# Performance work log

Measured on AMD Instinct MI355X. Metric: run time of the kernel, lower is better.

## Reference

```python
import jax, jax.numpy as jnp
import numpy as np

ALPHA, GAMMA = 0.25, 2.0
THR = 0.85            # soft_target_threshold
KL_EPS = 1e-6
FOCAL_EPS = 1e-8
VOC = 96              # len(vocab); index VOC is blank/pad


def setup_inputs() -> dict:
    key = jax.random.key(0)
    ks = jax.random.split(key, 6)
    bs, nq, n_pts, num_gt, L = 16, 200, 25, 32, 25
    return {
        "pred_logits": jax.random.normal(ks[0], (bs, nq, n_pts, 1), jnp.float32),
        "pred_ctrl_points": jax.random.uniform(ks[1], (bs, nq, n_pts, 2), jnp.float32),
        "pred_text_logits": jax.random.normal(ks[2], (bs, nq, n_pts, VOC + 1), jnp.float32),
        "tgt_ctrl_points": jax.random.uniform(ks[3], (bs, num_gt, n_pts, 2), jnp.float32),
        "tgt_texts": jax.random.randint(ks[4], (bs, num_gt, L), 0, VOC + 1),
        "centroids": jax.random.normal(ks[5], (VOC, 256), jnp.float32),
    }


def _cost_matrix(pred_logits, pred_ctrl_points, pred_text_logits,
                 tgt_ctrl_points, tgt_texts, centroids):
    bs, nq, n_pts, _ = pred_logits.shape
    num_gt = tgt_texts.shape[1]

    # ---- focal classification cost (mean over control points) ----
    out_prob = jax.nn.sigmoid(pred_logits.reshape(bs * nq, n_pts, -1))
    neg = (1.0 - ALPHA) * out_prob ** GAMMA * (-jnp.log1p(-(out_prob - FOCAL_EPS)))
    neg = (1.0 - ALPHA) * out_prob ** GAMMA * (-jnp.log(1.0 - out_prob + FOCAL_EPS))
    pos = ALPHA * (1.0 - out_prob) ** GAMMA * (-jnp.log(out_prob + FOCAL_EPS))
    cost_class = (pos[..., 0] - neg[..., 0]).mean(-1, keepdims=True)  # [bs*nq, 1]

    # ---- L1 cdist over flattened control points ----
    out_pts = pred_ctrl_points.reshape(bs * nq, n_pts * 2)
    tgt_pts = tgt_ctrl_points.reshape(bs * num_gt, n_pts * 2)
    cost_kpts = jnp.abs(out_pts[:, None, :] - tgt_pts[None, :, :]).sum(-1)  # [bs*nq, bs*num_gt]

    # ---- linguistic KL-div cost (per-batch block diagonal) ----
    probs = jax.nn.softmax(pred_text_logits, axis=-1)          # [bs,nq,n_pts,VOC+1]
    pred_avg = probs[..., :VOC].mean(axis=2)                   # [bs,nq,VOC]
    P = pred_avg + KL_EPS
    P = P / P.sum(-1, keepdims=True)
    logP = jnp.log(P)

    # soft target distribution per character (generate_soft_target_sequence)
    cn = centroids / jnp.linalg.norm(centroids, axis=-1, keepdims=True)
    soft_all = THR * jnp.eye(VOC, dtype=P.dtype) + (1.0 - THR) * jax.nn.softmax(cn @ cn.T, axis=-1)  # [VOC,VOC]

    mask = (tgt_texts != VOC)                                  # [bs,num_gt,L]
    lengths = mask.sum(-1)                                     # [bs,num_gt]
    per_char = soft_all[jnp.clip(tgt_texts, 0, VOC - 1)]       # [bs,num_gt,L,VOC]
    tgt_avg = (per_char * mask[..., None]).sum(2) / jnp.maximum(lengths, 1)[..., None].astype(P.dtype)
    T = tgt_avg + KL_EPS
    T = T / T.sum(-1, keepdims=True)                           # [bs,num_gt,VOC]

    # KL(T || P) = sum T*logT - sum T*logP, vectorized over (query, gt)
    kl = (T * jnp.log(T)).sum(-1)[:, None, :] - jnp.einsum('bqv,bgv->bqg', logP, T)  # [bs,nq,num_gt]
    kl = jnp.where(lengths[:, None, :] == 0, 100.0, kl)

    # place per-batch blocks on the diagonal of the global cost matrix
    eye = jnp.eye(bs, dtype=kl.dtype)
    cost_text = jnp.einsum('bqg,bc->bqcg', kl, eye).reshape(bs * nq, bs * num_gt)

    C = 1.0 * cost_class + 1.0 * cost_kpts + 1.0 * cost_text   # class/coord/text weights = 1
    return C.reshape(bs, nq, bs * num_gt)


def reference(pred_logits, pred_ctrl_points, pred_text_logits,
              tgt_ctrl_points, tgt_texts, centroids):
    return _cost_matrix(pred_logits, pred_ctrl_points, pred_text_logits,
                        tgt_ctrl_points, tgt_texts, centroids)
```

## Files before the change

kernel.cpp:

```cpp
#include <hip/hip_runtime.h>

#define BS 16
#define NQ 200
#define NPTS 25
#define VOC 96
#define VOCP1 97
#define NGT 32
#define LSEQ 25
#define NCOL (BS*NGT)
#define NBQ (BS*NQ)
#define KL_EPS 1e-6f
#define FOCAL_EPS 1e-8f

#define NB_LOGP NBQ
#define NB_SOFT VOC
#define NB_CDIST 400
#define NB_K1 (NB_LOGP + NB_SOFT + NB_CDIST)

__global__ __launch_bounds__(256) void K1(
        const float* __restrict__ pred_logits,
        const float* __restrict__ pred_ctrl,
        const float* __restrict__ pred_text_logits,
        const float* __restrict__ tgt_ctrl,
        const float* __restrict__ centroids,
        float* __restrict__ logP,
        float* __restrict__ soft,
        float* __restrict__ out)
{
    __shared__ __align__(16) float smem[64 * 52 * 2 + 64];
    const int tid = threadIdx.x;
    const int bid = blockIdx.x;

    if (bid < NB_LOGP) {
        const int bq = bid;
        float* s_buf    = smem;
        float* s_invden = smem + 2432;
        float* s_part   = smem + 2464;

        const float* tl = pred_text_logits + (size_t)bq * NPTS * VOCP1;
        for (int i = tid; i < NPTS * VOCP1; i += 256)
            s_buf[i] = __expf(tl[i]);
        __syncthreads();

        const int grp = tid >> 5, sub = tid & 31;
        for (int p = grp; p < NPTS; p += 8) {
            float s = 0.f;
            for (int v = sub; v < VOCP1; v += 32) s += s_buf[p * VOCP1 + v];
            #pragma unroll
            for (int off = 16; off; off >>= 1) s += __shfl_xor(s, off, 32);
            if (sub == 0) s_invden[p] = 1.0f / s;
        }
        __syncthreads();

        float avg = 0.f;
        if (tid < VOC) {
            float a = 0.f;
            #pragma unroll
            for (int p = 0; p < NPTS; p++)
                a += s_buf[p * VOCP1 + tid] * s_invden[p];
            avg = a * (1.0f / NPTS);
        }
        float s = avg;
        #pragma unroll
        for (int off = 32; off; off >>= 1) s += __shfl_xor(s, off);
        const int wave = tid >> 6, lane = tid & 63;
        if (lane == 0) s_part[wave] = s;
        __syncthreads();
        float denom = s_part[0] + s_part[1] + s_part[2] + s_part[3]
                    + (float)VOC * KL_EPS;
        if (tid < VOC)
            logP[(size_t)bq * VOC + tid] = __logf((avg + KL_EPS) / denom);

    } else if (bid < NB_LOGP + NB_SOFT) {
        const int i = bid - NB_LOGP;
        float4* s_c  = (float4*)smem;
        float* s_part = smem + 256;
        if (tid < 64)
            s_c[tid] = ((const float4*)(centroids + (size_t)i * 256))[tid];
        __syncthreads();

        float e = 0.f;
        if (tid < VOC) {
            float dij = 0.f, djj = 0.f, dii = 0.f;
            const float4* cj = (const float4*)(centroids + (size_t)tid * 256);
            #pragma unroll 4
            for (int k = 0; k < 64; k++) {
                float4 b = cj[k];
                float4 a = s_c[k];
                dij += a.x * b.x + a.y * b.y + a.z * b.z + a.w * b.w;
                djj += b.x * b.x + b.y * b.y + b.z * b.z + b.w * b.w;
                dii += a.x * a.x + a.y * a.y + a.z * a.z + a.w * a.w;
            }
            float sim = dij * rsqrtf(dii * djj);
            e = __expf(sim);
        }
        float s = e;
        #pragma unroll
        for (int off = 32; off; off >>= 1) s += __shfl_xor(s, off);
        const int wave = tid >> 6, lane = tid & 63;
        if (lane == 0) s_part[wave] = s;
        __syncthreads();
        float den = s_part[0] + s_part[1] + s_part[2] + s_part[3];
        if (tid < VOC) {
            float v = 0.15f * e / den;
            if (tid == i) v += 0.85f;
            soft[i * VOC + tid] = v;
        }

    } else {
        const int cid = bid - (NB_LOGP + NB_SOFT);
        const int r0  = (cid >> 3) * 64;
        const int c0  = (cid & 7) * 64;
        float (*s_p)[52] = (float (*)[52])smem;
        float (*s_t)[52] = (float (*)[52])(smem + 3328);
        float* s_cc = smem + 6656;

        const float* pg = pred_ctrl + (size_t)r0 * 50;
        const float* tg = tgt_ctrl + (size_t)c0 * 50;
        for (int i = tid; i < 64 * 50; i += 256) {
            int r = i / 50, d = i - r * 50;
            s_p[r][d] = pg[i];
            s_t[r][d] = tg[i];
        }
        {
            const int row4 = tid >> 2, q4 = tid & 3;
            float cc = 0.f;
            for (int p = q4; p < NPTS; p += 4) {
                float x  = pred_logits[(size_t)(r0 + row4) * NPTS + p];
                float pr = 1.f / (1.f + __expf(-x));
                float pos = 0.25f * (1.f - pr) * (1.f - pr) * (-__logf(pr + FOCAL_EPS));
                float neg = 0.75f * pr * pr * (-__logf(1.f - pr + FOCAL_EPS));
                cc += pos - neg;
            }
            cc += __shfl_xor(cc, 1, 4);
            cc += __shfl_xor(cc, 2, 4);
            if (q4 == 0) s_cc[row4] = cc * (1.0f / NPTS);
        }
        __syncthreads();

        const int tx = tid & 15;
        const int ty = tid >> 4;
        float acc[4][4];
        #pragma unroll
        for (int i = 0; i < 4; i++)
            #pragma unroll
            for (int j = 0; j < 4; j++) acc[i][j] = 0.f;

        #pragma unroll
        for (int k = 0; k < 48; k += 4) {
            float4 p[4], t[4];
            #pragma unroll
            for (int i = 0; i < 4; i++) p[i] = *(const float4*)&s_p[ty * 4 + i][k];
            #pragma unroll
            for (int j = 0; j < 4; j++) t[j] = *(const float4*)&s_t[tx + 16 * j][k];
            #pragma unroll
            for (int i = 0; i < 4; i++)
                #pragma unroll
                for (int j = 0; j < 4; j++)
                    acc[i][j] += fabsf(p[i].x - t[j].x) + fabsf(p[i].y - t[j].y)
                               + fabsf(p[i].z - t[j].z) + fabsf(p[i].w - t[j].w);
        }
        {
            float2 p[4], t[4];
            #pragma unroll
            for (int i = 0; i < 4; i++) p[i] = *(const float2*)&s_p[ty * 4 + i][48];
            #pragma unroll
            for (int j = 0; j < 4; j++) t[j] = *(const float2*)&s_t[tx + 16 * j][48];
            #pragma unroll
            for (int i = 0; i < 4; i++)
                #pragma unroll
                for (int j = 0; j < 4; j++)
                    acc[i][j] += fabsf(p[i].x - t[j].x) + fabsf(p[i].y - t[j].y);
        }

        #pragma unroll
        for (int i = 0; i < 4; i++) {
            const int row = ty * 4 + i;
            const float cc = s_cc[row];
            #pragma unroll
            for (int j = 0; j < 4; j++)
                out[(size_t)(r0 + row) * NCOL + c0 + tx + 16 * j] = acc[i][j] + cc;
        }
    }
}

__global__ __launch_bounds__(256) void K2(
        const int* __restrict__ tgt_texts,
        const float* __restrict__ soft,
        const float* __restrict__ logP,
        float* __restrict__ out)
{
    const int r0  = blockIdx.x * 8;
    const int b   = r0 / NQ;
    const int tid = threadIdx.x;
    __shared__ float s_soft[VOC * VOC];
    __shared__ int   s_chars[NGT * LSEQ];
    __shared__ float s_lp[8][VOC];
    __shared__ float s_Tt[VOC][NGT + 1];
    __shared__ float s_tl[NGT];
    __shared__ int   s_len[NGT];

    for (int i = tid; i < VOC * VOC / 4; i += 256)
        ((float4*)s_soft)[i] = ((const float4*)soft)[i];
    for (int i = tid; i < NGT * LSEQ; i += 256)
        s_chars[i] = tgt_texts[b * NGT * LSEQ + i];
    for (int i = tid; i < 8 * VOC; i += 256)
        s_lp[i / VOC][i % VOC] = logP[(size_t)r0 * VOC + i];
    __syncthreads();

    const int grp = tid >> 5, sub = tid & 31;
    for (int g = grp; g < NGT; g += 8) {
        int len = 0;
        float a0 = 0.f, a1 = 0.f, a2 = 0.f;
        for (int l = 0; l < LSEQ; l++) {
            int t = s_chars[g * LSEQ + l];
            if (t != VOC) {
                len++;
                const float* sr = s_soft + t * VOC;
                a0 += sr[sub]; a1 += sr[sub + 32]; a2 += sr[sub + 64];
            }
        }
        float inv = 1.f / (float)(len > 0 ? len : 1);
        a0 *= inv; a1 *= inv; a2 *= inv;
        float s = a0 + a1 + a2;
        #pragma unroll
        for (int off = 16; off; off >>= 1) s += __shfl_xor(s, off, 32);
        float denom = s + (float)VOC * KL_EPS;
        float t0 = (a0 + KL_EPS) / denom;
        float t1 = (a1 + KL_EPS) / denom;
        float t2 = (a2 + KL_EPS) / denom;
        s_Tt[sub][g]      = t0;
        s_Tt[sub + 32][g] = t1;
        s_Tt[sub + 64][g] = t2;
        float tl = t0 * __logf(t0) + t1 * __logf(t1) + t2 * __logf(t2);
        #pragma unroll
        for (int off = 16; off; off >>= 1) tl += __shfl_xor(tl, off, 32);
        if (sub == 0) { s_tl[g] = tl; s_len[g] = len; }
    }
    __syncthreads();

    const int g = tid & 31, rs = tid >> 5;
    float d = 0.f;
    #pragma unroll 8
    for (int v = 0; v < VOC; v++) d += s_lp[rs][v] * s_Tt[v][g];
    float val = (s_len[g] == 0) ? 100.f : (s_tl[g] - d);
    size_t o = (size_t)(r0 + rs) * NCOL + b * NGT + g;
    out[o] += val;
}

extern "C" void kernel_launch(void* const* d_in, const int* in_sizes, int n_in,
                              void* d_out, int out_size, void* d_ws, size_t ws_size,
                              hipStream_t stream) {
    const float* pred_logits = (const float*)d_in[0];
    const float* pred_ctrl   = (const float*)d_in[1];
    const float* pred_text   = (const float*)d_in[2];
    const float* tgt_ctrl    = (const float*)d_in[3];
    const int*   tgt_texts   = (const int*)d_in[4];
    const float* centroids   = (const float*)d_in[5];
    float* out = (float*)d_out;

    float* ws   = (float*)d_ws;
    float* logP = ws;
    float* soft = logP + (size_t)NBQ * VOC;

    K1<<<NB_K1, 256, 0, stream>>>(pred_logits, pred_ctrl, pred_text,
                                  tgt_ctrl, centroids, logP, soft, out);
    K2<<<400, 256, 0, stream>>>(tgt_texts, soft, logP, out);
}
```

Measured before the change: 126.0 us.

## Reorder K1 block roles, register-resident softmax averaging, read soft table from global

Moves the cdist blocks to the front of K1 so the heavy tiles get scheduled first. The per-query softmax-average path becomes wave-per-row register computation with shuffle reductions and a reciprocal intrinsic, replacing the shared-memory exp buffer and extra barriers. The denominator is derived analytically from the blank-column mass. K2 stops staging the 36KB soft table into LDS and reads it from global/L2, which frees LDS for occupancy but adds global-load latency in the inner loop.

```diff
diff --git a/kernel.cpp b/kernel.cpp
--- a/kernel.cpp
+++ b/kernel.cpp
@@ -12,10 +12,10 @@
 #define KL_EPS 1e-6f
 #define FOCAL_EPS 1e-8f
 
+#define NB_CDIST 400
+#define NB_SOFT VOC
 #define NB_LOGP NBQ
-#define NB_SOFT VOC
-#define NB_CDIST 400
-#define NB_K1 (NB_LOGP + NB_SOFT + NB_CDIST)
+#define NB_K1 (NB_CDIST + NB_SOFT + NB_LOGP)
 
 __global__ __launch_bounds__(256) void K1(
         const float* __restrict__ pred_logits,
@@ -31,48 +31,83 @@
     const int tid = threadIdx.x;
     const int bid = blockIdx.x;
 
-    if (bid < NB_LOGP) {
-        const int bq = bid;
-        float* s_buf    = smem;
-        float* s_invden = smem + 2432;
-        float* s_part   = smem + 2464;
-
-        const float* tl = pred_text_logits + (size_t)bq * NPTS * VOCP1;
-        for (int i = tid; i < NPTS * VOCP1; i += 256)
-            s_buf[i] = __expf(tl[i]);
-        __syncthreads();
-
-        const int grp = tid >> 5, sub = tid & 31;
-        for (int p = grp; p < NPTS; p += 8) {
-            float s = 0.f;
-            for (int v = sub; v < VOCP1; v += 32) s += s_buf[p * VOCP1 + v];
-            #pragma unroll
-            for (int off = 16; off; off >>= 1) s += __shfl_xor(s, off, 32);
-            if (sub == 0) s_invden[p] = 1.0f / s;
-        }
-        __syncthreads();
-
-        float avg = 0.f;
-        if (tid < VOC) {
-            float a = 0.f;
-            #pragma unroll
-            for (int p = 0; p < NPTS; p++)
-                a += s_buf[p * VOCP1 + tid] * s_invden[p];
-            avg = a * (1.0f / NPTS);
-        }
-        float s = avg;
-        #pragma unroll
-        for (int off = 32; off; off >>= 1) s += __shfl_xor(s, off);
-        const int wave = tid >> 6, lane = tid & 63;
-        if (lane == 0) s_part[wave] = s;
-        __syncthreads();
-        float denom = s_part[0] + s_part[1] + s_part[2] + s_part[3]
-                    + (float)VOC * KL_EPS;
-        if (tid < VOC)
-            logP[(size_t)bq * VOC + tid] = __logf((avg + KL_EPS) / denom);
-
-    } else if (bid < NB_LOGP + NB_SOFT) {
-        const int i = bid - NB_LOGP;
+    if (bid < NB_CDIST) {
+        const int cid = bid;
+        const int r0  = (cid >> 3) * 64;
+        const int c0  = (cid & 7) * 64;
+        float (*s_p)[52] = (float (*)[52])smem;
+        float (*s_t)[52] = (float (*)[52])(smem + 3328);
+        float* s_cc = smem + 6656;
+
+        const float* pg = pred_ctrl + (size_t)r0 * 50;
+        const float* tg = tgt_ctrl + (size_t)c0 * 50;
+        for (int i = tid; i < 64 * 50; i += 256) {
+            int r = i / 50, d = i - r * 50;
+            s_p[r][d] = pg[i];
+            s_t[r][d] = tg[i];
+        }
+        {
+            const int row4 = tid >> 2, q4 = tid & 3;
+            float cc = 0.f;
+            for (int p = q4; p < NPTS; p += 4) {
+                float x  = pred_logits[(size_t)(r0 + row4) * NPTS + p];
+                float pr = 1.f / (1.f + __expf(-x));
+                float pos = 0.25f * (1.f - pr) * (1.f - pr) * (-__logf(pr + FOCAL_EPS));
+                float neg = 0.75f * pr * pr * (-__logf(1.f - pr + FOCAL_EPS));
+                cc += pos - neg;
+            }
+            cc += __shfl_xor(cc, 1, 4);
+            cc += __shfl_xor(cc, 2, 4);
+            if (q4 == 0) s_cc[row4] = cc * (1.0f / NPTS);
+        }
+        __syncthreads();
+
+        const int tx = tid & 15;
+        const int ty = tid >> 4;
+        float acc[4][4];
+        #pragma unroll
+        for (int i = 0; i < 4; i++)
+            #pragma unroll
+            for (int j = 0; j < 4; j++) acc[i][j] = 0.f;
+
+        #pragma unroll
+        for (int k = 0; k < 48; k += 4) {
+            float4 p[4], t[4];
+            #pragma unroll
+            for (int i = 0; i < 4; i++) p[i] = *(const float4*)&s_p[ty * 4 + i][k];
+            #pragma unroll
+            for (int j = 0; j < 4; j++) t[j] = *(const float4*)&s_t[tx + 16 * j][k];
+            #pragma unroll
+            for (int i = 0; i < 4; i++)
+                #pragma unroll
+                for (int j = 0; j < 4; j++)
+                    acc[i][j] += fabsf(p[i].x - t[j].x) + fabsf(p[i].y - t[j].y)
+                               + fabsf(p[i].z - t[j].z) + fabsf(p[i].w - t[j].w);
+        }
+        {
+            float2 p[4], t[4];
+            #pragma unroll
+            for (int i = 0; i < 4; i++) p[i] = *(const float2*)&s_p[ty * 4 + i][48];
+            #pragma unroll
+            for (int j = 0; j < 4; j++) t[j] = *(const float2*)&s_t[tx + 16 * j][48];
+            #pragma unroll
+            for (int i = 0; i < 4; i++)
+                #pragma unroll
+                for (int j = 0; j < 4; j++)
+                    acc[i][j] += fabsf(p[i].x - t[j].x) + fabsf(p[i].y - t[j].y);
+        }
+
+        #pragma unroll
+        for (int i = 0; i < 4; i++) {
+            const int row = ty * 4 + i;
+            const float cc = s_cc[row];
+            #pragma unroll
+            for (int j = 0; j < 4; j++)
+                out[(size_t)(r0 + row) * NCOL + c0 + tx + 16 * j] = acc[i][j] + cc;
+        }
+
+    } else if (bid < NB_CDIST + NB_SOFT) {
+        const int i = bid - NB_CDIST;
         float4* s_c  = (float4*)smem;
         float* s_part = smem + 256;
         if (tid < 64)
@@ -108,78 +143,62 @@
         }
 
     } else {
-        const int cid = bid - (NB_LOGP + NB_SOFT);
-        const int r0  = (cid >> 3) * 64;
-        const int c0  = (cid & 7) * 64;
-        float (*s_p)[52] = (float (*)[52])smem;
-        float (*s_t)[52] = (float (*)[52])(smem + 3328);
-        float* s_cc = smem + 6656;
-
-        const float* pg = pred_ctrl + (size_t)r0 * 50;
-        const float* tg = tgt_ctrl + (size_t)c0 * 50;
-        for (int i = tid; i < 64 * 50; i += 256) {
-            int r = i / 50, d = i - r * 50;
-            s_p[r][d] = pg[i];
-            s_t[r][d] = tg[i];
-        }
-        {
-            const int row4 = tid >> 2, q4 = tid & 3;
-            float cc = 0.f;
-            for (int p = q4; p < NPTS; p += 4) {
-                float x  = pred_logits[(size_t)(r0 + row4) * NPTS + p];
-                float pr = 1.f / (1.f + __expf(-x));
-                float pos = 0.25f * (1.f - pr) * (1.f - pr) * (-__logf(pr + FOCAL_EPS));
-                float neg = 0.75f * pr * pr * (-__logf(1.f - pr + FOCAL_EPS));
-                cc += pos - neg;
-            }
-            cc += __shfl_xor(cc, 1, 4);
-            cc += __shfl_xor(cc, 2, 4);
-            if (q4 == 0) s_cc[row4] = cc * (1.0f / NPTS);
-        }
-        __syncthreads();
-
-        const int tx = tid & 15;
-        const int ty = tid >> 4;
-        float acc[4][4];
-        #pragma unroll
-        for (int i = 0; i < 4; i++)
-            #pragma unroll
-            for (int j = 0; j < 4; j++) acc[i][j] = 0.f;
-
-        #pragma unroll
-        for (int k = 0; k < 48; k += 4) {
-            float4 p[4], t[4];
-            #pragma unroll
-            for (int i = 0; i < 4; i++) p[i] = *(const float4*)&s_p[ty * 4 + i][k];
-            #pragma unroll
-            for (int j = 0; j < 4; j++) t[j] = *(const float4*)&s_t[tx + 16 * j][k];
-            #pragma unroll
-            for (int i = 0; i < 4; i++)
-                #pragma unroll
-                for (int j = 0; j < 4; j++)
-                    acc[i][j] += fabsf(p[i].x - t[j].x) + fabsf(p[i].y - t[j].y)
-                               + fabsf(p[i].z - t[j].z) + fabsf(p[i].w - t[j].w);
-        }
-        {
-            float2 p[4], t[4];
-            #pragma unroll
-            for (int i = 0; i < 4; i++) p[i] = *(const float2*)&s_p[ty * 4 + i][48];
-            #pragma unroll
-            for (int j = 0; j < 4; j++) t[j] = *(const float2*)&s_t[tx + 16 * j][48];
-            #pragma unroll
-            for (int i = 0; i < 4; i++)
-                #pragma unroll
-                for (int j = 0; j < 4; j++)
-                    acc[i][j] += fabsf(p[i].x - t[j].x) + fabsf(p[i].y - t[j].y);
-        }
-
-        #pragma unroll
-        for (int i = 0; i < 4; i++) {
-            const int row = ty * 4 + i;
-            const float cc = s_cc[row];
-            #pragma unroll
-            for (int j = 0; j < 4; j++)
-                out[(size_t)(r0 + row) * NCOL + c0 + tx + 16 * j] = acc[i][j] + cc;
+        const int bq   = bid - (NB_CDIST + NB_SOFT);
+        const int wave = tid >> 6, lane = tid & 63;
+        float* s_acc = smem;
+        float* s_p96 = smem + 388;
+
+        const float* tl = pred_text_logits + (size_t)bq * NPTS * VOCP1;
+
+        float e0[7], e1[7];
+        #pragma unroll
+        for (int k = 0; k < 6; k++) {
+            const float* row = tl + (size_t)(wave + 4 * k) * VOCP1;
+            e0[k] = row[lane];
+            e1[k] = (lane < 33) ? row[64 + lane] : 0.f;
+        }
+        if (wave == 0) {
+            const float* row = tl + (size_t)24 * VOCP1;
+            e0[6] = row[lane];
+            e1[6] = (lane < 33) ? row[64 + lane] : 0.f;
+        }
+
+        float acc0 = 0.f, acc1 = 0.f, acc96 = 0.f;
+        #pragma unroll
+        for (int k = 0; k < 6; k++) {
+            float a = __expf(e0[k]);
+            float b = (lane < 33) ? __expf(e1[k]) : 0.f;
+            float s = a + b;
+            #pragma unroll
+            for (int off = 32; off; off >>= 1) s += __shfl_xor(s, off);
+            float inv = __builtin_amdgcn_rcpf(s);
+            acc0  += a * inv;
+            acc1  += b * inv;
+            acc96 += __shfl(b, 32) * inv;
+        }
+        if (wave == 0) {
+            float a = __expf(e0[6]);
+            float b = (lane < 33) ? __expf(e1[6]) : 0.f;
+            float s = a + b;
+            #pragma unroll
+            for (int off = 32; off; off >>= 1) s += __shfl_xor(s, off);
+            float inv = __builtin_amdgcn_rcpf(s);
+            acc0  += a * inv;
+            acc1  += b * inv;
+            acc96 += __shfl(b, 32) * inv;
+        }
+
+        s_acc[wave * VOCP1 + lane] = acc0;
+        if (lane < 33) s_acc[wave * VOCP1 + 64 + lane] = acc1;
+        if (lane == 0) s_p96[wave] = acc96;
+        __syncthreads();
+
+        if (tid < VOC) {
+            float a = (s_acc[tid] + s_acc[VOCP1 + tid]
+                     + s_acc[2 * VOCP1 + tid] + s_acc[3 * VOCP1 + tid]) * (1.0f / NPTS);
+            float S96 = s_p96[0] + s_p96[1] + s_p96[2] + s_p96[3];
+            float denom = (25.0f - S96) * (1.0f / NPTS) + (float)VOC * KL_EPS;
+            logP[(size_t)bq * VOC + tid] = __logf((a + KL_EPS) / denom);
         }
     }
 }
@@ -193,15 +212,12 @@
     const int r0  = blockIdx.x * 8;
     const int b   = r0 / NQ;
     const int tid = threadIdx.x;
-    __shared__ float s_soft[VOC * VOC];
     __shared__ int   s_chars[NGT * LSEQ];
     __shared__ float s_lp[8][VOC];
     __shared__ float s_Tt[VOC][NGT + 1];
     __shared__ float s_tl[NGT];
     __shared__ int   s_len[NGT];
 
-    for (int i = tid; i < VOC * VOC / 4; i += 256)
-        ((float4*)s_soft)[i] = ((const float4*)soft)[i];
     for (int i = tid; i < NGT * LSEQ; i += 256)
         s_chars[i] = tgt_texts[b * NGT * LSEQ + i];
     for (int i = tid; i < 8 * VOC; i += 256)
@@ -216,7 +232,7 @@
             int t = s_chars[g * LSEQ + l];
             if (t != VOC) {
                 len++;
-                const float* sr = s_soft + t * VOC;
+                const float* sr = soft + t * VOC;
                 a0 += sr[sub]; a1 += sr[sub + 32]; a2 += sr[sub + 64];
             }
         }
```

New measurement: 115.6 us. -8.2%, faster.
